# Optimization experiments

Measured on AMD Instinct MI355X. Metric: run time of the kernel, lower is better.

The kernel has to match this reference:

```python
import jax, jax.numpy as jnp
import numpy as np

N = 100_000      # nodes
E = 1_600_000    # edges
F_IN = 128       # n_features == conv_dim1..3
F_OUT = 256      # concat_dim
G = 2000         # number of graphs in the batch
EPS = 1e-5       # BatchNorm eps


def _xavier(k, shape):
    fan_in, fan_out = shape[-2], shape[-1]
    lim = float(np.sqrt(6.0 / (fan_in + fan_out)))
    return jax.random.uniform(k, shape, jnp.float32, -lim, lim)


def setup_inputs() -> dict:
    key = jax.random.key(0)
    ks = jax.random.split(key, 8)
    x = jax.random.normal(ks[0], (N, F_IN), jnp.float32)
    edge_index = jax.random.randint(ks[1], (2, E), 0, N, dtype=jnp.int64)
    batch = jnp.sort(jax.random.randint(ks[2], (N,), 0, G, dtype=jnp.int64))
    # layers 1..5: F_IN -> F_IN (stacked), layer 6: F_IN -> F_OUT
    Wi = _xavier(ks[3], (5, F_IN, F_IN))   # ARMA init_weight per layer
    Wr = _xavier(ks[4], (5, F_IN, F_IN))   # ARMA root_weight per layer
    b = jnp.zeros((5, F_IN), jnp.float32)  # ARMA bias per layer
    g = jnp.ones((5, F_IN), jnp.float32)   # BN gamma
    be = jnp.zeros((5, F_IN), jnp.float32) # BN beta
    Wi6 = _xavier(ks[5], (F_IN, F_OUT))
    Wr6 = _xavier(ks[6], (F_IN, F_OUT))
    b6 = jnp.zeros((F_OUT,), jnp.float32)
    g6 = jnp.ones((F_OUT,), jnp.float32)
    be6 = jnp.zeros((F_OUT,), jnp.float32)
    return dict(x=x, edge_index=edge_index, batch=batch, Wi=Wi, Wr=Wr, b=b,
                g=g, be=be, Wi6=Wi6, Wr6=Wr6, b6=b6, g6=g6, be6=be6)


def _arma(x, norm, row, col, Wi_l, Wr_l, b_l):
    # ARMAConv (num_stacks=1, num_layers=1, act=ReLU):
    #   out = ReLU( A_norm @ (x W_init) + x W_root + b )
    h = x @ Wi_l                                           # [N, F_out]
    msg = h[row] * norm[:, None]                           # gather + scale, [E, F_out]
    agg = jax.ops.segment_sum(msg, col, num_segments=N)    # scatter-add
    return jax.nn.relu(agg + x @ Wr_l + b_l)


def _bn(x, gamma, beta):
    # BatchNorm1d, training mode (biased batch variance)
    mu = x.mean(axis=0)
    var = x.var(axis=0)
    return gamma * (x - mu) * jax.lax.rsqrt(var + EPS) + beta


def reference(x, edge_index, batch, Wi, Wr, b, g, be, Wi6, Wr6, b6, g6, be6):
    row, col = edge_index[0], edge_index[1]
    # gcn_norm without self loops: D^-1/2 A D^-1/2 edge weights
    deg = jax.ops.segment_sum(jnp.ones((E,), x.dtype), col, num_segments=N)
    dinv = jnp.where(deg > 0, jax.lax.rsqrt(deg), 0.0)
    norm = dinv[row] * dinv[col]                           # [E]

    h = x
    for l in range(5):  # fixed small layer count
        h = _arma(h, norm, row, col, Wi[l], Wr[l], b[l])   # outer F.relu is idempotent
        h = _bn(h, g[l], be[l])
    h = _arma(h, norm, row, col, Wi6, Wr6, b6)
    h = _bn(h, g6, be6)
    # global_add_pool over graph ids; dropout = identity (deterministic baseline)
    out = jax.ops.segment_sum(h, batch, num_segments=G)    # [G, F_OUT]
    return out
```

## Files before the change

kernel.cpp:

```cpp
#include <hip/hip_runtime.h>

#define Nn 100000
#define NP 100001
#define Ee 1600000
#define Gg 2000
#define EPSf 1e-5f

typedef unsigned short ushort_t;
typedef __attribute__((ext_vector_type(8))) short short8;
typedef __attribute__((ext_vector_type(4))) float f32x4;
typedef __attribute__((ext_vector_type(4))) unsigned u32x4;

__device__ inline float bf2f(unsigned int u) {
    union { unsigned int i; float f; } v; v.i = u << 16; return v.f;
}
__device__ inline unsigned short f2bf(float f) {
    unsigned int x = __float_as_uint(f);
    unsigned int r = (x + 0x7fffu + ((x >> 16) & 1u)) >> 16;
    return (unsigned short)r;
}
__device__ inline int ldidx(const void* a, int i, int i64) {
    return i64 ? (int)((const long long*)a)[i] : ((const int*)a)[i];
}
__device__ inline float ldflt(const void* p, long long i, int f32) {
    return f32 ? ((const float*)p)[i] : bf2f(((const ushort_t*)p)[i]);
}


__global__ void k_flags(const void* gones, const void* ei, int* flags) {
    if (threadIdx.x == 0 && blockIdx.x == 0) {
        unsigned w = *(const unsigned*)gones;
        flags[0] = (w == 0x3F800000u) ? 1 : 0;
        const int* e = (const int*)ei;
        int nz = 0;
        for (int i = 0; i < 256; i++) nz |= e[2 * i + 1];
        flags[1] = nz ? 0 : 1;
    }
}


__global__ void k_hist(const void* __restrict__ ei, int* __restrict__ deg, const int* __restrict__ flags) {
    int i = blockIdx.x * 256 + threadIdx.x;
    if (i < Ee) {
        int c = ldidx(ei, Ee + i, flags[1]);
        atomicAdd(&deg[c], 1);
    }
}

__global__ void k_dinv(const int* __restrict__ deg, float* __restrict__ dinv) {
    int i = blockIdx.x * 256 + threadIdx.x;
    if (i < Nn) { int d = deg[i]; dinv[i] = d > 0 ? rsqrtf((float)d) : 0.f; }
}

__global__ void k_scan1(const int* __restrict__ deg, int* __restrict__ off, int* __restrict__ part) {
    __shared__ int sh[1024];
    int i = blockIdx.x * 1024 + threadIdx.x;
    int v = (i < Nn) ? ((deg[i] + 3) & ~3) : 0;
    sh[threadIdx.x] = v;
    __syncthreads();
    for (int ofs = 1; ofs < 1024; ofs <<= 1) {
        int t = 0;
        if ((int)threadIdx.x >= ofs) t = sh[threadIdx.x - ofs];
        __syncthreads();
        sh[threadIdx.x] += t;
        __syncthreads();
    }
    if (i < Nn) off[i] = sh[threadIdx.x] - v;
    if (threadIdx.x == 1023) part[blockIdx.x] = sh[1023];
}

__global__ void k_scan2(int* part, int nb) {
    if (threadIdx.x == 0 && blockIdx.x == 0) {
        int run = 0;
        for (int i = 0; i < nb; i++) { int t = part[i]; part[i] = run; run += t; }
        part[nb] = run;
    }
}

__global__ void k_scan3(int* __restrict__ off, const int* __restrict__ part, int* __restrict__ cursor) {
    int i = blockIdx.x * 256 + threadIdx.x;
    if (i < Nn) {
        int v = off[i] + part[i >> 10];
        off[i] = v;
        cursor[i] = v;
    }
    if (i == 0) off[Nn] = part[98];
}

__global__ void k_fillp(const void* __restrict__ ei, int* __restrict__ cursor,
                        int* __restrict__ srcS, const int* __restrict__ flags) {
    int range = blockIdx.x & 7;
    int e = (blockIdx.x >> 3) * 256 + threadIdx.x;
    if (e < Ee) {
        int i64 = flags[1];
        int c = ldidx(ei, Ee + e, i64);
        if (c >= range * 12500 && c < (range + 1) * 12500) {
            int r = ldidx(ei, e, i64);
            int p = atomicAdd(&cursor[c], 1);
            srcS[p] = r;
        }
    }
}

__global__ void k_pad(const int* __restrict__ cursor, const int* __restrict__ off,
                      int* __restrict__ srcS) {
    int i = blockIdx.x * 256 + threadIdx.x;
    if (i < Nn) {
        int e = off[i + 1];
        for (int p = cursor[i]; p < e; p++) srcS[p] = Nn;
    }
}

__global__ void k_zrow(ushort_t* __restrict__ Hi) {
    int t = threadIdx.x;
    int fc = t >> 4, j = t & 15;
    Hi[((size_t)fc * NP + Nn) * 16 + j] = 0;
}

__global__ void k_cvtp(const void* b, const void* b6, const void* g, const void* g6,
                       const void* be, const void* be6,
                       float* __restrict__ biasF, float* __restrict__ gF,
                       float* __restrict__ beF, const int* __restrict__ flags) {
    int i = blockIdx.x * 256 + threadIdx.x;
    if (i >= 2688) return;
    int grp = i / 896, r = i - grp * 896;
    int f32 = flags[0];
    const void* srcs[6] = { b, b6, g, g6, be, be6 };
    float* dsts[3] = { biasF, gF, beF };
    const void* s = (r < 640) ? srcs[grp * 2] : srcs[grp * 2 + 1];
    int idx = (r < 640) ? r : r - 640;
    dsts[grp][r] = ldflt(s, idx, f32);
}

__global__ void k_cvtx(const void* __restrict__ x, ushort_t* __restrict__ xq, const int* __restrict__ flags) {
    int node = blockIdx.x * 256 + threadIdx.x;
    int fc = blockIdx.y;
    if (node < Nn) {
        union { ushort_t u[16]; u32x4 v[2]; } t;
        if (flags[0]) {
            const float* p = (const float*)x + (size_t)node * 128 + fc * 16;
#pragma unroll
            for (int j = 0; j < 16; j++) t.u[j] = f2bf(p[j]);
        } else {
            const ushort_t* p = (const ushort_t*)x + (size_t)node * 128 + fc * 16;
#pragma unroll
            for (int j = 0; j < 16; j++) t.u[j] = p[j];
        }
        u32x4* d = (u32x4*)(xq + ((size_t)fc * Nn + node) * 16);
        d[0] = t.v[0]; d[1] = t.v[1];
    }
}

__global__ void k_pack(const void* __restrict__ Wi, const void* __restrict__ Wr,
                       const void* __restrict__ Wi6, const void* __restrict__ Wr6,
                       ushort_t* __restrict__ Bp, const int* __restrict__ flags) {
    int idx = blockIdx.x * 256 + threadIdx.x;
    if (idx >= 229376) return;
    int f32 = flags[0];
    if (idx < 163840) {
        int l = idx / 32768, rem = idx - l * 32768;
        int kg = rem / 2048, rem2 = rem - kg * 2048;
        int n = rem2 / 8, j = rem2 - n * 8;
        int k = kg * 8 + j;
        float v = (n < 128) ? ldflt(Wi, (l * 128 + k) * 128 + n, f32)
                            : ldflt(Wr, (l * 128 + k) * 128 + (n - 128), f32);
        Bp[idx] = f2bf(v);
    } else {
        int idx2 = idx - 163840;
        int kg = idx2 / 4096, rem2 = idx2 - kg * 4096;
        int n = rem2 / 8, j = rem2 - n * 8;
        int k = kg * 8 + j;
        float v = (n < 256) ? ldflt(Wi6, k * 256 + n, f32) : ldflt(Wr6, k * 256 + (n - 256), f32);
        Bp[idx] = f2bf(v);
    }
}

__global__ void k_fold(const ushort_t* __restrict__ Bp, const float* __restrict__ stat,
                       const float* __restrict__ gamma, const float* __restrict__ beta,
                       const float* __restrict__ bias,
                       ushort_t* __restrict__ Bp2, float* __restrict__ hcorr, int ncat) {
    __shared__ float red[128];
    int n = blockIdx.x, k = threadIdx.x;
    int fhalf = ncat >> 1;
    float mu = stat[k] * (1.f / Nn);
    float var = stat[128 + k] * (1.f / Nn) - mu * mu;
    float rs = rsqrtf(var + EPSf);
    float s = gamma[k] * rs;
    float h = beta[k] - s * mu;
    size_t idx = ((size_t)(k >> 3) * ncat + n) * 8 + (k & 7);
    float w = bf2f(Bp[idx]);
    Bp2[idx] = f2bf(w * s);
    red[k] = h * w;
    __syncthreads();
    for (int m = 64; m > 0; m >>= 1) { if (k < m) red[k] += red[k + m]; __syncthreads(); }
    if (k == 0) hcorr[n] = red[0] + (n >= fhalf ? bias[n - fhalf] : 0.f);
}

__global__ void k_h0(const float* __restrict__ bias, float* __restrict__ hc, int ncat) {
    int n = blockIdx.x * 256 + threadIdx.x;
    if (n < ncat) hc[n] = n >= (ncat >> 1) ? bias[n - (ncat >> 1)] : 0.f;
}


__global__ __launch_bounds__(256) void k_gemm(
        const ushort_t* __restrict__ Aq,
        const ushort_t* __restrict__ Bp, const float* __restrict__ hcorr,
        const float* __restrict__ dinv,
        ushort_t* __restrict__ Hi, ushort_t* __restrict__ yq, int ncat) {
    __shared__ ushort_t stage[32 * 264];
    const int tid = threadIdx.x, lane = tid & 63, wid = tid >> 6;
    const int q = lane >> 4, l15 = lane & 15;
    const int fhalf = ncat >> 1;
    const int colW = blockIdx.y * 256 + wid * 64;
    const int row0 = blockIdx.x * 64;

    short8 bfr[4][4];
    float hc[4];
#pragma unroll
    for (int kk = 0; kk < 4; kk++) {
        int kg = kk * 4 + q;
#pragma unroll
        for (int ct = 0; ct < 4; ct++)
            bfr[kk][ct] = *(const short8*)(Bp + ((size_t)kg * ncat + colW + ct * 16 + l15) * 8);
    }
#pragma unroll
    for (int ct = 0; ct < 4; ct++) hc[ct] = hcorr[colW + ct * 16 + l15];

    f32x4 acc[4][4];
    f32x4 z; z.x = 0.f; z.y = 0.f; z.z = 0.f; z.w = 0.f;
#pragma unroll
    for (int rt = 0; rt < 4; rt++)
#pragma unroll
        for (int ct = 0; ct < 4; ct++) acc[rt][ct] = z;

#pragma unroll
    for (int kk = 0; kk < 4; kk++) {
        int kg = kk * 4 + q;
        const ushort_t* ap = Aq + (size_t)(kg >> 1) * Nn * 16 + (kg & 1) * 8;
        short8 af[4];
#pragma unroll
        for (int rt = 0; rt < 4; rt++) {
            int node = row0 + rt * 16 + l15;
            if (node >= Nn) node = Nn - 1;
            af[rt] = *(const short8*)(ap + (size_t)node * 16);
        }
#pragma unroll
        for (int rt = 0; rt < 4; rt++)
#pragma unroll
            for (int ct = 0; ct < 4; ct++)
                acc[rt][ct] = __builtin_amdgcn_mfma_f32_16x16x32_bf16(af[rt], bfr[kk][ct], acc[rt][ct], 0, 0, 0);
    }

#pragma unroll
    for (int half = 0; half < 2; half++) {
        __syncthreads();
#pragma unroll
        for (int ct = 0; ct < 4; ct++) {
            int lcol = wid * 64 + ct * 16 + l15;
            bool isHi = (blockIdx.y * 256 + lcol) < fhalf;
#pragma unroll
            for (int rt2 = 0; rt2 < 2; rt2++) {
                int rt = half * 2 + rt2;
#pragma unroll
                for (int r = 0; r < 4; r++) {
                    int grow = row0 + rt * 16 + q * 4 + r;
                    int gr = grow < Nn ? grow : 0;
                    float v = acc[rt][ct][r] + hc[ct];
                    if (isHi) v *= dinv[gr];
                    stage[(rt2 * 16 + q * 4 + r) * 264 + lcol] = f2bf(v);
                }
            }
        }
        __syncthreads();
        for (int chunk = tid; chunk < 512; chunk += 256) {
            int cg = chunk & 15, rl = chunk >> 4;
            int node = row0 + half * 32 + rl;
            if (node < Nn) {
                int gc0 = blockIdx.y * 256 + cg * 16;
                const u32x4* sp = (const u32x4*)&stage[rl * 264 + cg * 16];
                u32x4 v0 = sp[0], v1 = sp[1];
                ushort_t* dst = (gc0 < fhalf)
                    ? Hi + ((size_t)(gc0 >> 4) * NP + node) * 16
                    : yq + ((size_t)((gc0 - fhalf) >> 4) * Nn + node) * 16;
                u32x4* dp = (u32x4*)dst;
                dp[0] = v0; dp[1] = v1;
            }
        }
    }
}


__global__ __launch_bounds__(256) void k_agg8(const int* __restrict__ off, const int* __restrict__ src,
                                              const float* __restrict__ dinv, const unsigned* __restrict__ Hi2,
                                              unsigned* __restrict__ yq, float* __restrict__ stat,
                                              int F, int fcbase) {
    const int tid = threadIdx.x;
    const int w = tid >> 6, lane = tid & 63;
    const int sub = lane >> 3, fl = lane & 7;
    const int e2 = (fl >> 1) & 3;
    const int h  = fl & 1;
    const int fc = fcbase + (blockIdx.x & 7);
    const int T = blockIdx.x >> 3;
    const char* __restrict__ gbase = (const char*)Hi2 + (size_t)fc * ((size_t)NP * 32) + h * 16;

    float stS[8], stQ[8];
#pragma unroll
    for (int j = 0; j < 8; j++) { stS[j] = 0.f; stQ[j] = 0.f; }

#pragma unroll
    for (int pass = 0; pass < 4; pass++) {
        int node = T * 128 + pass * 32 + w * 8 + sub;
        bool valid = node < Nn;
        int p0 = 0, p1 = 0;
        if (valid) { p0 = off[node]; p1 = off[node + 1]; }
        float a[8];
#pragma unroll
        for (int j = 0; j < 8; j++) a[j] = 0.f;
        int p = p0;
        for (; p + 15 < p1; p += 16) {
            int s0 = src[p + e2];
            int s1 = src[p + 4 + e2];
            int s2 = src[p + 8 + e2];
            int s3 = src[p + 12 + e2];
            u32x4 g0 = *(const u32x4*)(gbase + (size_t)((unsigned)s0 << 5));
            u32x4 g1 = *(const u32x4*)(gbase + (size_t)((unsigned)s1 << 5));
            u32x4 g2 = *(const u32x4*)(gbase + (size_t)((unsigned)s2 << 5));
            u32x4 g3 = *(const u32x4*)(gbase + (size_t)((unsigned)s3 << 5));
#pragma unroll
            for (int d = 0; d < 4; d++) {
                a[2*d]   += bf2f(g0[d] & 0xffffu); a[2*d+1] += bf2f(g0[d] >> 16);
                a[2*d]   += bf2f(g1[d] & 0xffffu); a[2*d+1] += bf2f(g1[d] >> 16);
                a[2*d]   += bf2f(g2[d] & 0xffffu); a[2*d+1] += bf2f(g2[d] >> 16);
                a[2*d]   += bf2f(g3[d] & 0xffffu); a[2*d+1] += bf2f(g3[d] >> 16);
            }
        }
        if (p + 7 < p1) {
            int s0 = src[p + e2];
            int s1 = src[p + 4 + e2];
            u32x4 g0 = *(const u32x4*)(gbase + (size_t)((unsigned)s0 << 5));
            u32x4 g1 = *(const u32x4*)(gbase + (size_t)((unsigned)s1 << 5));
#pragma unroll
            for (int d = 0; d < 4; d++) {
                a[2*d]   += bf2f(g0[d] & 0xffffu); a[2*d+1] += bf2f(g0[d] >> 16);
                a[2*d]   += bf2f(g1[d] & 0xffffu); a[2*d+1] += bf2f(g1[d] >> 16);
            }
            p += 8;
        }
        if (p < p1) {
            int s0 = src[p + e2];
            u32x4 g0 = *(const u32x4*)(gbase + (size_t)((unsigned)s0 << 5));
#pragma unroll
            for (int d = 0; d < 4; d++) {
                a[2*d]   += bf2f(g0[d] & 0xffffu); a[2*d+1] += bf2f(g0[d] >> 16);
            }
        }
#pragma unroll
        for (int j = 0; j < 8; j++) {
            a[j] += __shfl_xor(a[j], 2, 64);
            a[j] += __shfl_xor(a[j], 4, 64);
        }
        if (valid && fl < 2) {
            float dv = dinv[node];
            u32x4* yp = (u32x4*)(yq + ((size_t)fc * Nn + node) * 8 + h * 4);
            u32x4 uv = *yp;
#pragma unroll
            for (int d = 0; d < 4; d++) {
                float vlo = fmaxf(bf2f(uv[d] & 0xffffu) + dv * a[2*d],   0.f);
                float vhi = fmaxf(bf2f(uv[d] >> 16)     + dv * a[2*d+1], 0.f);
                uv[d] = (unsigned)f2bf(vlo) | ((unsigned)f2bf(vhi) << 16);
                stS[2*d]   += vlo; stQ[2*d]   += vlo * vlo;
                stS[2*d+1] += vhi; stQ[2*d+1] += vhi * vhi;
            }
            *yp = uv;
        }
    }
#pragma unroll
    for (int j = 0; j < 8; j++) {
        stS[j] += __shfl_xor(stS[j], 8, 64);
        stQ[j] += __shfl_xor(stQ[j], 8, 64);
        stS[j] += __shfl_xor(stS[j], 16, 64);
        stQ[j] += __shfl_xor(stQ[j], 16, 64);
        stS[j] += __shfl_xor(stS[j], 32, 64);
        stQ[j] += __shfl_xor(stQ[j], 32, 64);
    }
    __shared__ float red[4][2][8][2];
    if (lane < 2) {
#pragma unroll
        for (int j = 0; j < 8; j++) {
            red[w][lane][j][0] = stS[j];
            red[w][lane][j][1] = stQ[j];
        }
    }
    __syncthreads();
    if (tid < 32) {
        int hh = tid >> 4, r = tid & 15, j = r >> 1, m = r & 1;
        float s = red[0][hh][j][m] + red[1][hh][j][m] + red[2][hh][j][m] + red[3][hh][j][m];
        int f = fc * 16 + hh * 8 + j;
        atomicAdd(&stat[m * F + f], s);
    }
}


__device__ inline int lb(const void* a, int n, int key, int i64) {
    int lo = 0, hi = n;
    while (lo < hi) { int mid = (lo + hi) >> 1; if (ldidx(a, mid, i64) < key) lo = mid + 1; else hi = mid; }
    return lo;
}

__global__ void k_pool(const ushort_t* __restrict__ y6q, const float* __restrict__ stat,
                       const float* __restrict__ g6, const float* __restrict__ be6,
                       const void* __restrict__ batch, void* __restrict__ out,
                       const int* __restrict__ flags) {
    int g = blockIdx.x;
    int f = threadIdx.x;
    int i64 = flags[1];
    int start = lb(batch, Nn, g, i64);
    int end = lb(batch, Nn, g + 1, i64);
    const ushort_t* yp = y6q + (size_t)(f >> 4) * Nn * 16 + (f & 15);
    float s = 0.f;
    for (int n = start; n < end; n++) s += bf2f(yp[(size_t)n * 16]);
    int cnt = end - start;
    float mu = stat[f] * (1.f / Nn);
    float var = stat[256 + f] * (1.f / Nn) - mu * mu;
    float rs = rsqrtf(var + EPSf);
    float val = g6[f] * rs * (s - (float)cnt * mu) + (float)cnt * be6[f];
    if (flags[0]) ((float*)out)[(size_t)g * 256 + f] = val;
    else          ((ushort_t*)out)[(size_t)g * 256 + f] = f2bf(val);
}


extern "C" void kernel_launch(void* const* d_in, const int* in_sizes, int n_in,
                              void* d_out, int out_size, void* d_ws, size_t ws_size,
                              hipStream_t stream) {
    const void* x    = d_in[0];
    const void* ei   = d_in[1];
    const void* batch= d_in[2];
    const void* Wi   = d_in[3];
    const void* Wr   = d_in[4];
    const void* b    = d_in[5];
    const void* g    = d_in[6];
    const void* be   = d_in[7];
    const void* Wi6  = d_in[8];
    const void* Wr6  = d_in[9];
    const void* b6   = d_in[10];
    const void* g6   = d_in[11];
    const void* be6  = d_in[12];

    char* p = (char*)d_ws;
    auto alloc = [&](size_t bytes) { char* r = p; p += (bytes + 511) & ~(size_t)511; return r; };
    ushort_t* HiB  = (ushort_t*)alloc((size_t)NP * 256 * 2);
    ushort_t* xq   = (ushort_t*)alloc((size_t)Nn * 128 * 2);
    ushort_t* yAq  = (ushort_t*)alloc((size_t)Nn * 128 * 2);
    ushort_t* yBq  = (ushort_t*)alloc((size_t)Nn * 128 * 2);
    ushort_t* y6q  = (ushort_t*)alloc((size_t)Nn * 256 * 2);
    int* srcS      = (int*)alloc(((size_t)Ee + 4 * Nn + 64) * 4);
    int* off       = (int*)alloc((size_t)(Nn + 1) * 4);
    int* cursor    = (int*)alloc((size_t)Nn * 4);
    int* deg       = (int*)alloc((size_t)Nn * 4);
    float* dinv    = (float*)alloc((size_t)Nn * 4);
    int* part      = (int*)alloc(128 * 4);
    float* statsA  = (float*)alloc(6 * 512 * 4);
    ushort_t* Bp   = (ushort_t*)alloc(229376 * 2);
    ushort_t* Bp2  = (ushort_t*)alloc(65536 * 2);
    float* hcorrA  = (float*)alloc(512 * 4);
    int* flags     = (int*)alloc(2 * 4);
    float* biasF   = (float*)alloc(896 * 4);
    float* gF      = (float*)alloc(896 * 4);
    float* beF     = (float*)alloc(896 * 4);
    const unsigned* Hi2 = (const unsigned*)HiB;

    const int AGG_GRID = 782 * 8;
    const int GEMM_GRID = 1563;

    k_flags<<<1, 64, 0, stream>>>(g, ei, flags);
    k_cvtp<<<11, 256, 0, stream>>>(b, b6, g, g6, be, be6, biasF, gF, beF, flags);

    hipMemsetAsync(deg, 0, (size_t)Nn * 4, stream);
    hipMemsetAsync(statsA, 0, 6 * 512 * 4, stream);
    k_hist<<<6250, 256, 0, stream>>>(ei, deg, flags);
    k_dinv<<<391, 256, 0, stream>>>(deg, dinv);
    k_scan1<<<98, 1024, 0, stream>>>(deg, off, part);
    k_scan2<<<1, 64, 0, stream>>>(part, 98);
    k_scan3<<<391, 256, 0, stream>>>(off, part, cursor);
    k_fillp<<<50000, 256, 0, stream>>>(ei, cursor, srcS, flags);
    k_pad<<<391, 256, 0, stream>>>(cursor, off, srcS);
    k_zrow<<<1, 256, 0, stream>>>(HiB);
    k_pack<<<896, 256, 0, stream>>>(Wi, Wr, Wi6, Wr6, Bp, flags);
    k_cvtx<<<dim3(391, 8), 256, 0, stream>>>(x, xq, flags);
    k_h0<<<1, 256, 0, stream>>>(biasF, hcorrA, 256);

    k_gemm<<<dim3(GEMM_GRID, 1), 256, 0, stream>>>(xq, Bp, hcorrA, dinv, HiB, yAq, 256);
    k_agg8<<<AGG_GRID, 256, 0, stream>>>(off, srcS, dinv, Hi2, (unsigned*)yAq, statsA, 128, 0);
    k_fold<<<256, 128, 0, stream>>>(Bp + 32768, statsA, gF, beF, biasF + 128, Bp2, hcorrA, 256);

    k_gemm<<<dim3(GEMM_GRID, 1), 256, 0, stream>>>(yAq, Bp2, hcorrA, dinv, HiB, yBq, 256);
    k_agg8<<<AGG_GRID, 256, 0, stream>>>(off, srcS, dinv, Hi2, (unsigned*)yBq, statsA + 512, 128, 0);
    k_fold<<<256, 128, 0, stream>>>(Bp + 65536, statsA + 512, gF + 128, beF + 128, biasF + 256, Bp2, hcorrA, 256);

    k_gemm<<<dim3(GEMM_GRID, 1), 256, 0, stream>>>(yBq, Bp2, hcorrA, dinv, HiB, yAq, 256);
    k_agg8<<<AGG_GRID, 256, 0, stream>>>(off, srcS, dinv, Hi2, (unsigned*)yAq, statsA + 1024, 128, 0);
    k_fold<<<256, 128, 0, stream>>>(Bp + 98304, statsA + 1024, gF + 256, beF + 256, biasF + 384, Bp2, hcorrA, 256);

    k_gemm<<<dim3(GEMM_GRID, 1), 256, 0, stream>>>(yAq, Bp2, hcorrA, dinv, HiB, yBq, 256);
    k_agg8<<<AGG_GRID, 256, 0, stream>>>(off, srcS, dinv, Hi2, (unsigned*)yBq, statsA + 1536, 128, 0);
    k_fold<<<256, 128, 0, stream>>>(Bp + 131072, statsA + 1536, gF + 384, beF + 384, biasF + 512, Bp2, hcorrA, 256);

    k_gemm<<<dim3(GEMM_GRID, 1), 256, 0, stream>>>(yBq, Bp2, hcorrA, dinv, HiB, yAq, 256);
    k_agg8<<<AGG_GRID, 256, 0, stream>>>(off, srcS, dinv, Hi2, (unsigned*)yAq, statsA + 2048, 128, 0);
    k_fold<<<512, 128, 0, stream>>>(Bp + 163840, statsA + 2048, gF + 512, beF + 512, biasF + 640, Bp2, hcorrA, 512);

    k_gemm<<<dim3(GEMM_GRID, 2), 256, 0, stream>>>(yAq, Bp2, hcorrA, dinv, HiB, y6q, 512);
    k_agg8<<<AGG_GRID, 256, 0, stream>>>(off, srcS, dinv, Hi2, (unsigned*)y6q, statsA + 2560, 256, 0);
    k_agg8<<<AGG_GRID, 256, 0, stream>>>(off, srcS, dinv, Hi2, (unsigned*)y6q, statsA + 2560, 256, 8);
    k_pool<<<Gg, 256, 0, stream>>>(y6q, statsA + 2560, gF + 640, be6 ? beF + 640 : beF + 640, batch, d_out, flags);
}
```

Before: 1.145 ms.

## Sort nodes by degree bucket to balance aggregation warp workloads

Adds a counting sort of nodes into 64 degree buckets, highest degree first, and builds the CSR in that sorted slot order. The aggregation kernel then walks slots and maps each back to its node through a permutation. The goal is to cut divergence inside the 8-node groups of a wavefront, where lanes with short edge lists sit idle waiting for neighbours with long ones. In exchange there are three extra setup kernels, an indirect perm lookup in every aggregation pass, and node writes that are no longer coalesced.

After: 1.182 ms. 3.3% more time.

```diff
diff --git a/kernel.cpp b/kernel.cpp
--- a/kernel.cpp
+++ b/kernel.cpp
@@ -5,6 +5,8 @@
 #define Ee 1600000
 #define Gg 2000
 #define EPSf 1e-5f
+#define NBLK 391
+#define BH_STRIDE 400
 
 typedef unsigned short ushort_t;
 typedef __attribute__((ext_vector_type(8))) short short8;
@@ -25,6 +27,7 @@
 __device__ inline float ldflt(const void* p, long long i, int f32) {
     return f32 ? ((const float*)p)[i] : bf2f(((const ushort_t*)p)[i]);
 }
+__device__ inline int dbucket(int d) { int b = (d + 3) >> 2; return b > 63 ? 63 : b; }
 
 
 __global__ void k_flags(const void* gones, const void* ei, int* flags) {
@@ -52,10 +55,60 @@
     if (i < Nn) { int d = deg[i]; dinv[i] = d > 0 ? rsqrtf((float)d) : 0.f; }
 }
 
-__global__ void k_scan1(const int* __restrict__ deg, int* __restrict__ off, int* __restrict__ part) {
+
+__global__ void k_dhist(const int* __restrict__ deg, int* __restrict__ bhT) {
+    __shared__ int hist[64];
+    int tid = threadIdx.x, blk = blockIdx.x;
+    if (tid < 64) hist[tid] = 0;
+    __syncthreads();
+    int i = blk * 256 + tid;
+    if (i < Nn) atomicAdd(&hist[dbucket(deg[i])], 1);
+    __syncthreads();
+    if (tid < 64) bhT[tid * BH_STRIDE + blk] = hist[tid];
+}
+
+__global__ void k_bscan(int* __restrict__ bhT, int* __restrict__ baseG) {
+    __shared__ int tot[64];
+    __shared__ int base[64];
+    int t = threadIdx.x;
+    int run = 0;
+    for (int k = 0; k < NBLK; k++) {
+        int v = bhT[t * BH_STRIDE + k];
+        bhT[t * BH_STRIDE + k] = run;
+        run += v;
+    }
+    tot[t] = run;
+    __syncthreads();
+    if (t == 0) {
+        int r = 0;
+        for (int b = 63; b >= 0; b--) { base[b] = r; r += tot[b]; }
+    }
+    __syncthreads();
+    baseG[t] = base[t];
+}
+
+__global__ void k_dfill(const int* __restrict__ deg, const float* __restrict__ dinv,
+                        const int* __restrict__ bhT, const int* __restrict__ baseG,
+                        int* __restrict__ perm, int* __restrict__ degS, float* __restrict__ dinvS) {
+    __shared__ int cur[64];
+    int tid = threadIdx.x, blk = blockIdx.x;
+    if (tid < 64) cur[tid] = bhT[tid * BH_STRIDE + blk] + baseG[tid];
+    __syncthreads();
+    int i = blk * 256 + tid;
+    if (i < Nn) {
+        int d = deg[i];
+        int b = dbucket(d);
+        int pos = atomicAdd(&cur[b], 1);
+        perm[pos] = i;
+        degS[pos] = (d + 3) & ~3;
+        dinvS[pos] = dinv[i];
+    }
+}
+
+__global__ void k_scan1(const int* __restrict__ degS, int* __restrict__ off, int* __restrict__ part) {
     __shared__ int sh[1024];
     int i = blockIdx.x * 1024 + threadIdx.x;
-    int v = (i < Nn) ? ((deg[i] + 3) & ~3) : 0;
+    int v = (i < Nn) ? degS[i] : 0;
     sh[threadIdx.x] = v;
     __syncthreads();
     for (int ofs = 1; ofs < 1024; ofs <<= 1) {
@@ -77,14 +130,15 @@
     }
 }
 
-__global__ void k_scan3(int* __restrict__ off, const int* __restrict__ part, int* __restrict__ cursor) {
+__global__ void k_scan3(int* __restrict__ offS, const int* __restrict__ part,
+                        const int* __restrict__ perm, int* __restrict__ cursor) {
     int i = blockIdx.x * 256 + threadIdx.x;
     if (i < Nn) {
-        int v = off[i] + part[i >> 10];
-        off[i] = v;
-        cursor[i] = v;
-    }
-    if (i == 0) off[Nn] = part[98];
+        int v = offS[i] + part[i >> 10];
+        offS[i] = v;
+        cursor[perm[i]] = v;
+    }
+    if (i == 0) offS[Nn] = part[98];
 }
 
 __global__ void k_fillp(const void* __restrict__ ei, int* __restrict__ cursor,
@@ -102,12 +156,13 @@
     }
 }
 
-__global__ void k_pad(const int* __restrict__ cursor, const int* __restrict__ off,
-                      int* __restrict__ srcS) {
+__global__ void k_pad(const int* __restrict__ cursor, const int* __restrict__ offS,
+                      const int* __restrict__ perm, int* __restrict__ srcS) {
     int i = blockIdx.x * 256 + threadIdx.x;
     if (i < Nn) {
-        int e = off[i + 1];
-        for (int p = cursor[i]; p < e; p++) srcS[p] = Nn;
+        int node = perm[i];
+        int e = offS[i + 1];
+        for (int p = cursor[node]; p < e; p++) srcS[p] = Nn;
     }
 }
 
@@ -290,8 +345,9 @@
 }
 
 
-__global__ __launch_bounds__(256) void k_agg8(const int* __restrict__ off, const int* __restrict__ src,
-                                              const float* __restrict__ dinv, const unsigned* __restrict__ Hi2,
+__global__ __launch_bounds__(256) void k_agg8(const int* __restrict__ offS, const int* __restrict__ src,
+                                              const int* __restrict__ perm,
+                                              const float* __restrict__ dinvS, const unsigned* __restrict__ Hi2,
                                               unsigned* __restrict__ yq, float* __restrict__ stat,
                                               int F, int fcbase) {
     const int tid = threadIdx.x;
@@ -309,10 +365,10 @@
 
 #pragma unroll
     for (int pass = 0; pass < 4; pass++) {
-        int node = T * 128 + pass * 32 + w * 8 + sub;
-        bool valid = node < Nn;
+        int slot = T * 128 + pass * 32 + w * 8 + sub;
+        bool valid = slot < Nn;
         int p0 = 0, p1 = 0;
-        if (valid) { p0 = off[node]; p1 = off[node + 1]; }
+        if (valid) { p0 = offS[slot]; p1 = offS[slot + 1]; }
         float a[8];
 #pragma unroll
         for (int j = 0; j < 8; j++) a[j] = 0.f;
@@ -360,7 +416,8 @@
             a[j] += __shfl_xor(a[j], 4, 64);
         }
         if (valid && fl < 2) {
-            float dv = dinv[node];
+            int node = perm[slot];
+            float dv = dinvS[slot];
             u32x4* yp = (u32x4*)(yq + ((size_t)fc * Nn + node) * 8 + h * 4);
             u32x4 uv = *yp;
 #pragma unroll
@@ -454,7 +511,7 @@
     ushort_t* yBq  = (ushort_t*)alloc((size_t)Nn * 128 * 2);
     ushort_t* y6q  = (ushort_t*)alloc((size_t)Nn * 256 * 2);
     int* srcS      = (int*)alloc(((size_t)Ee + 4 * Nn + 64) * 4);
-    int* off       = (int*)alloc((size_t)(Nn + 1) * 4);
+    int* offS      = (int*)alloc((size_t)(Nn + 1) * 4);
     int* cursor    = (int*)alloc((size_t)Nn * 4);
     int* deg       = (int*)alloc((size_t)Nn * 4);
     float* dinv    = (float*)alloc((size_t)Nn * 4);
@@ -467,6 +524,11 @@
     float* biasF   = (float*)alloc(896 * 4);
     float* gF      = (float*)alloc(896 * 4);
     float* beF     = (float*)alloc(896 * 4);
+    int* perm      = (int*)alloc((size_t)Nn * 4);
+    int* degS      = (int*)alloc((size_t)Nn * 4);
+    float* dinvS   = (float*)alloc((size_t)Nn * 4);
+    int* bhT       = (int*)alloc(64 * BH_STRIDE * 4);
+    int* baseG     = (int*)alloc(64 * 4);
     const unsigned* Hi2 = (const unsigned*)HiB;
 
     const int AGG_GRID = 782 * 8;
@@ -479,38 +541,41 @@
     hipMemsetAsync(statsA, 0, 6 * 512 * 4, stream);
     k_hist<<<6250, 256, 0, stream>>>(ei, deg, flags);
     k_dinv<<<391, 256, 0, stream>>>(deg, dinv);
-    k_scan1<<<98, 1024, 0, stream>>>(deg, off, part);
+    k_dhist<<<NBLK, 256, 0, stream>>>(deg, bhT);
+    k_bscan<<<1, 64, 0, stream>>>(bhT, baseG);
+    k_dfill<<<NBLK, 256, 0, stream>>>(deg, dinv, bhT, baseG, perm, degS, dinvS);
+    k_scan1<<<98, 1024, 0, stream>>>(degS, offS, part);
     k_scan2<<<1, 64, 0, stream>>>(part, 98);
-    k_scan3<<<391, 256, 0, stream>>>(off, part, cursor);
+    k_scan3<<<391, 256, 0, stream>>>(offS, part, perm, cursor);
     k_fillp<<<50000, 256, 0, stream>>>(ei, cursor, srcS, flags);
-    k_pad<<<391, 256, 0, stream>>>(cursor, off, srcS);
+    k_pad<<<391, 256, 0, stream>>>(cursor, offS, perm, srcS);
     k_zrow<<<1, 256, 0, stream>>>(HiB);
     k_pack<<<896, 256, 0, stream>>>(Wi, Wr, Wi6, Wr6, Bp, flags);
     k_cvtx<<<dim3(391, 8), 256, 0, stream>>>(x, xq, flags);
     k_h0<<<1, 256, 0, stream>>>(biasF, hcorrA, 256);
 
     k_gemm<<<dim3(GEMM_GRID, 1), 256, 0, stream>>>(xq, Bp, hcorrA, dinv, HiB, yAq, 256);
-    k_agg8<<<AGG_GRID, 256, 0, stream>>>(off, srcS, dinv, Hi2, (unsigned*)yAq, statsA, 128, 0);
+    k_agg8<<<AGG_GRID, 256, 0, stream>>>(offS, srcS, perm, dinvS, Hi2, (unsigned*)yAq, statsA, 128, 0);
     k_fold<<<256, 128, 0, stream>>>(Bp + 32768, statsA, gF, beF, biasF + 128, Bp2, hcorrA, 256);
 
     k_gemm<<<dim3(GEMM_GRID, 1), 256, 0, stream>>>(yAq, Bp2, hcorrA, dinv, HiB, yBq, 256);
-    k_agg8<<<AGG_GRID, 256, 0, stream>>>(off, srcS, dinv, Hi2, (unsigned*)yBq, statsA + 512, 128, 0);
+    k_agg8<<<AGG_GRID, 256, 0, stream>>>(offS, srcS, perm, dinvS, Hi2, (unsigned*)yBq, statsA + 512, 128, 0);
     k_fold<<<256, 128, 0, stream>>>(Bp + 65536, statsA + 512, gF + 128, beF + 128, biasF + 256, Bp2, hcorrA, 256);
 
     k_gemm<<<dim3(GEMM_GRID, 1), 256, 0, stream>>>(yBq, Bp2, hcorrA, dinv, HiB, yAq, 256);
-    k_agg8<<<AGG_GRID, 256, 0, stream>>>(off, srcS, dinv, Hi2, (unsigned*)yAq, statsA + 1024, 128, 0);
+    k_agg8<<<AGG_GRID, 256, 0, stream>>>(offS, srcS, perm, dinvS, Hi2, (unsigned*)yAq, statsA + 1024, 128, 0);
     k_fold<<<256, 128, 0, stream>>>(Bp + 98304, statsA + 1024, gF + 256, beF + 256, biasF + 384, Bp2, hcorrA, 256);
 
     k_gemm<<<dim3(GEMM_GRID, 1), 256, 0, stream>>>(yAq, Bp2, hcorrA, dinv, HiB, yBq, 256);
-    k_agg8<<<AGG_GRID, 256, 0, stream>>>(off, srcS, dinv, Hi2, (unsigned*)yBq, statsA + 1536, 128, 0);
+    k_agg8<<<AGG_GRID, 256, 0, stream>>>(offS, srcS, perm, dinvS, Hi2, (unsigned*)yBq, statsA + 1536, 128, 0);
     k_fold<<<256, 128, 0, stream>>>(Bp + 131072, statsA + 1536, gF + 384, beF + 384, biasF + 512, Bp2, hcorrA, 256);
 
     k_gemm<<<dim3(GEMM_GRID, 1), 256, 0, stream>>>(yBq, Bp2, hcorrA, dinv, HiB, yAq, 256);
-    k_agg8<<<AGG_GRID, 256, 0, stream>>>(off, srcS, dinv, Hi2, (unsigned*)yAq, statsA + 2048, 128, 0);
+    k_agg8<<<AGG_GRID, 256, 0, stream>>>(offS, srcS, perm, dinvS, Hi2, (unsigned*)yAq, statsA + 2048, 128, 0);
     k_fold<<<512, 128, 0, stream>>>(Bp + 163840, statsA + 2048, gF + 512, beF + 512, biasF + 640, Bp2, hcorrA, 512);
 
     k_gemm<<<dim3(GEMM_GRID, 2), 256, 0, stream>>>(yAq, Bp2, hcorrA, dinv, HiB, y6q, 512);
-    k_agg8<<<AGG_GRID, 256, 0, stream>>>(off, srcS, dinv, Hi2, (unsigned*)y6q, statsA + 2560, 256, 0);
-    k_agg8<<<AGG_GRID, 256, 0, stream>>>(off, srcS, dinv, Hi2, (unsigned*)y6q, statsA + 2560, 256, 8);
-    k_pool<<<Gg, 256, 0, stream>>>(y6q, statsA + 2560, gF + 640, be6 ? beF + 640 : beF + 640, batch, d_out, flags);
-}
+    k_agg8<<<AGG_GRID, 256, 0, stream>>>(offS, srcS, perm, dinvS, Hi2, (unsigned*)y6q, statsA + 2560, 256, 0);
+    k_agg8<<<AGG_GRID, 256, 0, stream>>>(offS, srcS, perm, dinvS, Hi2, (unsigned*)y6q, statsA + 2560, 256, 8);
+    k_pool<<<Gg, 256, 0, stream>>>(y6q, statsA + 2560, gF + 640, beF + 640, batch, d_out, flags);
+}
```

## Aggregate before transform in final layer to halve gather width

Applied to the files above, without the earlier changes.

For the last layer (128→256), the change reorders the algebra: it aggregates the 128-wide input features (pre-scaled by dinv) over neighbors, then runs one K=256 GEMM over [aggregated, root] inputs. This avoids gathering 256-wide transformed features twice, since the old path needed two agg8 passes. The BN shift term is handled through a per-node dsn factor times a folded hm vector, and the BN statistics are now accumulated inside the new GEMM epilogue. It adds a dsn precompute pass, an extra Hs buffer write in layer 5's aggregation, and some changes to the fold and pack layout.

Result: faster. 1.098 ms (-4.1%).

```diff
diff --git a/kernel.cpp b/kernel.cpp
--- a/kernel.cpp
+++ b/kernel.cpp
@@ -50,6 +50,7 @@
 __global__ void k_dinv(const int* __restrict__ deg, float* __restrict__ dinv) {
     int i = blockIdx.x * 256 + threadIdx.x;
     if (i < Nn) { int d = deg[i]; dinv[i] = d > 0 ? rsqrtf((float)d) : 0.f; }
+    if (i == Nn) dinv[i] = 0.f;
 }
 
 __global__ void k_scan1(const int* __restrict__ deg, int* __restrict__ off, int* __restrict__ part) {
@@ -111,10 +112,22 @@
     }
 }
 
-__global__ void k_zrow(ushort_t* __restrict__ Hi) {
+__global__ void k_dsn(const int* __restrict__ off, const int* __restrict__ src,
+                      const float* __restrict__ dinv, float* __restrict__ dsn) {
+    int i = blockIdx.x * 256 + threadIdx.x;
+    if (i < Nn) {
+        int p0 = off[i], p1 = off[i + 1];
+        float s = 0.f;
+        for (int p = p0; p < p1; p++) s += dinv[src[p]];
+        dsn[i] = dinv[i] * s;
+    }
+}
+
+__global__ void k_zrow(ushort_t* __restrict__ Hi, ushort_t* __restrict__ Hs) {
     int t = threadIdx.x;
     int fc = t >> 4, j = t & 15;
     Hi[((size_t)fc * NP + Nn) * 16 + j] = 0;
+    if (t < 128) Hs[((size_t)(t >> 4) * NP + Nn) * 16 + (t & 15)] = 0;
 }
 
 __global__ void k_cvtp(const void* b, const void* b6, const void* g, const void* g6,
@@ -167,10 +180,10 @@
         Bp[idx] = f2bf(v);
     } else {
         int idx2 = idx - 163840;
-        int kg = idx2 / 4096, rem2 = idx2 - kg * 4096;
+        int kg = idx2 / 2048, rem2 = idx2 - kg * 2048;
         int n = rem2 / 8, j = rem2 - n * 8;
         int k = kg * 8 + j;
-        float v = (n < 256) ? ldflt(Wi6, k * 256 + n, f32) : ldflt(Wr6, k * 256 + (n - 256), f32);
+        float v = (k < 128) ? ldflt(Wi6, k * 256 + n, f32) : ldflt(Wr6, (k - 128) * 256 + n, f32);
         Bp[idx] = f2bf(v);
     }
 }
@@ -196,6 +209,34 @@
     if (k == 0) hcorr[n] = red[0] + (n >= fhalf ? bias[n - fhalf] : 0.f);
 }
 
+__global__ void k_fold5(const ushort_t* __restrict__ Braw, const float* __restrict__ stat,
+                        const float* __restrict__ gamma, const float* __restrict__ beta,
+                        const float* __restrict__ bias,
+                        ushort_t* __restrict__ Bf, float* __restrict__ hm, float* __restrict__ hcorr) {
+    __shared__ float redA[128];
+    __shared__ float redB[128];
+    int n = blockIdx.x, k = threadIdx.x;
+    float mu = stat[k] * (1.f / Nn);
+    float var = stat[128 + k] * (1.f / Nn) - mu * mu;
+    float rs = rsqrtf(var + EPSf);
+    float s = gamma[k] * rs;
+    float t = beta[k] - s * mu;
+    size_t idxWi = ((size_t)(k >> 3) * 256 + n) * 8 + (k & 7);
+    size_t idxWr = ((size_t)(16 + (k >> 3)) * 256 + n) * 8 + (k & 7);
+    float wi = bf2f(Braw[idxWi]);
+    float wr = bf2f(Braw[idxWr]);
+    Bf[idxWi] = f2bf(wi * s);
+    Bf[idxWr] = f2bf(wr * s);
+    redA[k] = t * wi;
+    redB[k] = t * wr;
+    __syncthreads();
+    for (int m = 64; m > 0; m >>= 1) {
+        if (k < m) { redA[k] += redA[k + m]; redB[k] += redB[k + m]; }
+        __syncthreads();
+    }
+    if (k == 0) { hm[n] = redA[0]; hcorr[n] = redB[0] + bias[n]; }
+}
+
 __global__ void k_h0(const float* __restrict__ bias, float* __restrict__ hc, int ncat) {
     int n = blockIdx.x * 256 + threadIdx.x;
     if (n < ncat) hc[n] = n >= (ncat >> 1) ? bias[n - (ncat >> 1)] : 0.f;
@@ -211,7 +252,7 @@
     const int tid = threadIdx.x, lane = tid & 63, wid = tid >> 6;
     const int q = lane >> 4, l15 = lane & 15;
     const int fhalf = ncat >> 1;
-    const int colW = blockIdx.y * 256 + wid * 64;
+    const int colW = wid * 64;
     const int row0 = blockIdx.x * 64;
 
     short8 bfr[4][4];
@@ -257,7 +298,7 @@
 #pragma unroll
         for (int ct = 0; ct < 4; ct++) {
             int lcol = wid * 64 + ct * 16 + l15;
-            bool isHi = (blockIdx.y * 256 + lcol) < fhalf;
+            bool isHi = lcol < fhalf;
 #pragma unroll
             for (int rt2 = 0; rt2 < 2; rt2++) {
                 int rt = half * 2 + rt2;
@@ -276,7 +317,7 @@
             int cg = chunk & 15, rl = chunk >> 4;
             int node = row0 + half * 32 + rl;
             if (node < Nn) {
-                int gc0 = blockIdx.y * 256 + cg * 16;
+                int gc0 = cg * 16;
                 const u32x4* sp = (const u32x4*)&stage[rl * 264 + cg * 16];
                 u32x4 v0 = sp[0], v1 = sp[1];
                 ushort_t* dst = (gc0 < fhalf)
@@ -290,10 +331,105 @@
 }
 
 
+__global__ __launch_bounds__(256) void k_gemm5(
+        const ushort_t* __restrict__ aggH, const ushort_t* __restrict__ y4,
+        const ushort_t* __restrict__ Bp, const float* __restrict__ hcorr,
+        const float* __restrict__ hm, const float* __restrict__ dsn,
+        ushort_t* __restrict__ y6, float* __restrict__ stat) {
+    __shared__ ushort_t stage[32 * 264];
+    const int tid = threadIdx.x, lane = tid & 63, wid = tid >> 6;
+    const int q = lane >> 4, l15 = lane & 15;
+    const int colW = wid * 64;
+    const int row0 = blockIdx.x * 64;
+
+    float hc[4], hmv[4];
+#pragma unroll
+    for (int ct = 0; ct < 4; ct++) {
+        hc[ct] = hcorr[colW + ct * 16 + l15];
+        hmv[ct] = hm[colW + ct * 16 + l15];
+    }
+
+    f32x4 acc[4][4];
+    f32x4 z; z.x = 0.f; z.y = 0.f; z.z = 0.f; z.w = 0.f;
+#pragma unroll
+    for (int rt = 0; rt < 4; rt++)
+#pragma unroll
+        for (int ct = 0; ct < 4; ct++) acc[rt][ct] = z;
+
+#pragma unroll
+    for (int kk = 0; kk < 8; kk++) {
+        int kg = kk * 4 + q;
+        const ushort_t* ap = ((kg < 16)
+            ? aggH + (size_t)(kg >> 1) * ((size_t)Nn * 16)
+            : y4 + (size_t)((kg - 16) >> 1) * ((size_t)Nn * 16)) + (kg & 1) * 8;
+        short8 af[4];
+#pragma unroll
+        for (int rt = 0; rt < 4; rt++) {
+            int node = row0 + rt * 16 + l15;
+            if (node >= Nn) node = Nn - 1;
+            af[rt] = *(const short8*)(ap + (size_t)node * 16);
+        }
+        short8 bf[4];
+#pragma unroll
+        for (int ct = 0; ct < 4; ct++)
+            bf[ct] = *(const short8*)(Bp + ((size_t)kg * 256 + colW + ct * 16 + l15) * 8);
+#pragma unroll
+        for (int rt = 0; rt < 4; rt++)
+#pragma unroll
+            for (int ct = 0; ct < 4; ct++)
+                acc[rt][ct] = __builtin_amdgcn_mfma_f32_16x16x32_bf16(af[rt], bf[ct], acc[rt][ct], 0, 0, 0);
+    }
+
+    float sS = 0.f, sQ = 0.f;
+#pragma unroll
+    for (int half = 0; half < 2; half++) {
+        __syncthreads();
+#pragma unroll
+        for (int ct = 0; ct < 4; ct++) {
+            int lcol = wid * 64 + ct * 16 + l15;
+#pragma unroll
+            for (int rt2 = 0; rt2 < 2; rt2++) {
+                int rt = half * 2 + rt2;
+#pragma unroll
+                for (int r = 0; r < 4; r++) {
+                    int grow = row0 + rt * 16 + q * 4 + r;
+                    int gr = grow < Nn ? grow : 0;
+                    float v = acc[rt][ct][r] + hc[ct] + dsn[gr] * hmv[ct];
+                    v = fmaxf(v, 0.f);
+                    stage[(rt2 * 16 + q * 4 + r) * 264 + lcol] = f2bf(v);
+                }
+            }
+        }
+        __syncthreads();
+        for (int chunk = tid; chunk < 512; chunk += 256) {
+            int cg = chunk & 15, rl = chunk >> 4;
+            int node = row0 + half * 32 + rl;
+            if (node < Nn) {
+                int gc0 = cg * 16;
+                const u32x4* sp = (const u32x4*)&stage[rl * 264 + cg * 16];
+                u32x4 v0 = sp[0], v1 = sp[1];
+                ushort_t* dst = y6 + ((size_t)(gc0 >> 4) * Nn + node) * 16;
+                u32x4* dp = (u32x4*)dst;
+                dp[0] = v0; dp[1] = v1;
+            }
+        }
+        for (int rl = 0; rl < 32; rl++) {
+            int node = row0 + half * 32 + rl;
+            if (node < Nn) {
+                float v = bf2f(stage[rl * 264 + tid]);
+                sS += v; sQ += v * v;
+            }
+        }
+    }
+    atomicAdd(&stat[tid], sS);
+    atomicAdd(&stat[256 + tid], sQ);
+}
+
+
 __global__ __launch_bounds__(256) void k_agg8(const int* __restrict__ off, const int* __restrict__ src,
                                               const float* __restrict__ dinv, const unsigned* __restrict__ Hi2,
                                               unsigned* __restrict__ yq, float* __restrict__ stat,
-                                              int F, int fcbase) {
+                                              int F, int fcbase, unsigned* __restrict__ HsOut) {
     const int tid = threadIdx.x;
     const int w = tid >> 6, lane = tid & 63;
     const int sub = lane >> 3, fl = lane & 7;
@@ -363,15 +499,18 @@
             float dv = dinv[node];
             u32x4* yp = (u32x4*)(yq + ((size_t)fc * Nn + node) * 8 + h * 4);
             u32x4 uv = *yp;
+            u32x4 hs;
 #pragma unroll
             for (int d = 0; d < 4; d++) {
                 float vlo = fmaxf(bf2f(uv[d] & 0xffffu) + dv * a[2*d],   0.f);
                 float vhi = fmaxf(bf2f(uv[d] >> 16)     + dv * a[2*d+1], 0.f);
                 uv[d] = (unsigned)f2bf(vlo) | ((unsigned)f2bf(vhi) << 16);
+                hs[d] = (unsigned)f2bf(vlo * dv) | ((unsigned)f2bf(vhi * dv) << 16);
                 stS[2*d]   += vlo; stQ[2*d]   += vlo * vlo;
                 stS[2*d+1] += vhi; stQ[2*d+1] += vhi * vhi;
             }
             *yp = uv;
+            if (HsOut) *(u32x4*)(HsOut + ((size_t)fc * NP + node) * 8 + h * 4) = hs;
         }
     }
 #pragma unroll
@@ -397,6 +536,82 @@
         float s = red[0][hh][j][m] + red[1][hh][j][m] + red[2][hh][j][m] + red[3][hh][j][m];
         int f = fc * 16 + hh * 8 + j;
         atomicAdd(&stat[m * F + f], s);
+    }
+}
+
+
+__global__ __launch_bounds__(256) void k_agg5(const int* __restrict__ off, const int* __restrict__ src,
+                                              const float* __restrict__ dinv, const unsigned* __restrict__ Hs2,
+                                              unsigned* __restrict__ aggH) {
+    const int tid = threadIdx.x;
+    const int w = tid >> 6, lane = tid & 63;
+    const int sub = lane >> 3, fl = lane & 7;
+    const int e2 = (fl >> 1) & 3;
+    const int h  = fl & 1;
+    const int fc = blockIdx.x & 7;
+    const int T = blockIdx.x >> 3;
+    const char* __restrict__ gbase = (const char*)Hs2 + (size_t)fc * ((size_t)NP * 32) + h * 16;
+
+#pragma unroll
+    for (int pass = 0; pass < 4; pass++) {
+        int node = T * 128 + pass * 32 + w * 8 + sub;
+        bool valid = node < Nn;
+        int p0 = 0, p1 = 0;
+        if (valid) { p0 = off[node]; p1 = off[node + 1]; }
+        float a[8];
+#pragma unroll
+        for (int j = 0; j < 8; j++) a[j] = 0.f;
+        int p = p0;
+        for (; p + 15 < p1; p += 16) {
+            int s0 = src[p + e2];
+            int s1 = src[p + 4 + e2];
+            int s2 = src[p + 8 + e2];
+            int s3 = src[p + 12 + e2];
+            u32x4 g0 = *(const u32x4*)(gbase + (size_t)((unsigned)s0 << 5));
+            u32x4 g1 = *(const u32x4*)(gbase + (size_t)((unsigned)s1 << 5));
+            u32x4 g2 = *(const u32x4*)(gbase + (size_t)((unsigned)s2 << 5));
+            u32x4 g3 = *(const u32x4*)(gbase + (size_t)((unsigned)s3 << 5));
+#pragma unroll
+            for (int d = 0; d < 4; d++) {
+                a[2*d]   += bf2f(g0[d] & 0xffffu); a[2*d+1] += bf2f(g0[d] >> 16);
+                a[2*d]   += bf2f(g1[d] & 0xffffu); a[2*d+1] += bf2f(g1[d] >> 16);
+                a[2*d]   += bf2f(g2[d] & 0xffffu); a[2*d+1] += bf2f(g2[d] >> 16);
+                a[2*d]   += bf2f(g3[d] & 0xffffu); a[2*d+1] += bf2f(g3[d] >> 16);
+            }
+        }
+        if (p + 7 < p1) {
+            int s0 = src[p + e2];
+            int s1 = src[p + 4 + e2];
+            u32x4 g0 = *(const u32x4*)(gbase + (size_t)((unsigned)s0 << 5));
+            u32x4 g1 = *(const u32x4*)(gbase + (size_t)((unsigned)s1 << 5));
+#pragma unroll
+            for (int d = 0; d < 4; d++) {
+                a[2*d]   += bf2f(g0[d] & 0xffffu); a[2*d+1] += bf2f(g0[d] >> 16);
+                a[2*d]   += bf2f(g1[d] & 0xffffu); a[2*d+1] += bf2f(g1[d] >> 16);
+            }
+            p += 8;
+        }
+        if (p < p1) {
+            int s0 = src[p + e2];
+            u32x4 g0 = *(const u32x4*)(gbase + (size_t)((unsigned)s0 << 5));
+#pragma unroll
+            for (int d = 0; d < 4; d++) {
+                a[2*d]   += bf2f(g0[d] & 0xffffu); a[2*d+1] += bf2f(g0[d] >> 16);
+            }
+        }
+#pragma unroll
+        for (int j = 0; j < 8; j++) {
+            a[j] += __shfl_xor(a[j], 2, 64);
+            a[j] += __shfl_xor(a[j], 4, 64);
+        }
+        if (valid && fl < 2) {
+            float dv = dinv[node];
+            u32x4 o;
+#pragma unroll
+            for (int d = 0; d < 4; d++)
+                o[d] = (unsigned)f2bf(dv * a[2*d]) | ((unsigned)f2bf(dv * a[2*d+1]) << 16);
+            *(u32x4*)(aggH + ((size_t)fc * Nn + node) * 8 + h * 4) = o;
+        }
     }
 }
 
@@ -449,6 +664,8 @@
     char* p = (char*)d_ws;
     auto alloc = [&](size_t bytes) { char* r = p; p += (bytes + 511) & ~(size_t)511; return r; };
     ushort_t* HiB  = (ushort_t*)alloc((size_t)NP * 256 * 2);
+    ushort_t* HsB  = (ushort_t*)alloc((size_t)NP * 128 * 2);
+    ushort_t* aggH = (ushort_t*)alloc((size_t)Nn * 128 * 2);
     ushort_t* xq   = (ushort_t*)alloc((size_t)Nn * 128 * 2);
     ushort_t* yAq  = (ushort_t*)alloc((size_t)Nn * 128 * 2);
     ushort_t* yBq  = (ushort_t*)alloc((size_t)Nn * 128 * 2);
@@ -457,12 +674,15 @@
     int* off       = (int*)alloc((size_t)(Nn + 1) * 4);
     int* cursor    = (int*)alloc((size_t)Nn * 4);
     int* deg       = (int*)alloc((size_t)Nn * 4);
-    float* dinv    = (float*)alloc((size_t)Nn * 4);
+    float* dinv    = (float*)alloc((size_t)(Nn + 1) * 4);
+    float* dsn     = (float*)alloc((size_t)Nn * 4);
     int* part      = (int*)alloc(128 * 4);
     float* statsA  = (float*)alloc(6 * 512 * 4);
     ushort_t* Bp   = (ushort_t*)alloc(229376 * 2);
     ushort_t* Bp2  = (ushort_t*)alloc(65536 * 2);
     float* hcorrA  = (float*)alloc(512 * 4);
+    float* hm6     = (float*)alloc(256 * 4);
+    float* hcorr6  = (float*)alloc(256 * 4);
     int* flags     = (int*)alloc(2 * 4);
     float* biasF   = (float*)alloc(896 * 4);
     float* gF      = (float*)alloc(896 * 4);
@@ -478,39 +698,39 @@
     hipMemsetAsync(deg, 0, (size_t)Nn * 4, stream);
     hipMemsetAsync(statsA, 0, 6 * 512 * 4, stream);
     k_hist<<<6250, 256, 0, stream>>>(ei, deg, flags);
-    k_dinv<<<391, 256, 0, stream>>>(deg, dinv);
+    k_dinv<<<392, 256, 0, stream>>>(deg, dinv);
     k_scan1<<<98, 1024, 0, stream>>>(deg, off, part);
     k_scan2<<<1, 64, 0, stream>>>(part, 98);
     k_scan3<<<391, 256, 0, stream>>>(off, part, cursor);
     k_fillp<<<50000, 256, 0, stream>>>(ei, cursor, srcS, flags);
     k_pad<<<391, 256, 0, stream>>>(cursor, off, srcS);
-    k_zrow<<<1, 256, 0, stream>>>(HiB);
+    k_dsn<<<391, 256, 0, stream>>>(off, srcS, dinv, dsn);
+    k_zrow<<<1, 256, 0, stream>>>(HiB, HsB);
     k_pack<<<896, 256, 0, stream>>>(Wi, Wr, Wi6, Wr6, Bp, flags);
     k_cvtx<<<dim3(391, 8), 256, 0, stream>>>(x, xq, flags);
     k_h0<<<1, 256, 0, stream>>>(biasF, hcorrA, 256);
 
     k_gemm<<<dim3(GEMM_GRID, 1), 256, 0, stream>>>(xq, Bp, hcorrA, dinv, HiB, yAq, 256);
-    k_agg8<<<AGG_GRID, 256, 0, stream>>>(off, srcS, dinv, Hi2, (unsigned*)yAq, statsA, 128, 0);
+    k_agg8<<<AGG_GRID, 256, 0, stream>>>(off, srcS, dinv, Hi2, (unsigned*)yAq, statsA, 128, 0, nullptr);
     k_fold<<<256, 128, 0, stream>>>(Bp + 32768, statsA, gF, beF, biasF + 128, Bp2, hcorrA, 256);
 
     k_gemm<<<dim3(GEMM_GRID, 1), 256, 0, stream>>>(yAq, Bp2, hcorrA, dinv, HiB, yBq, 256);
-    k_agg8<<<AGG_GRID, 256, 0, stream>>>(off, srcS, dinv, Hi2, (unsigned*)yBq, statsA + 512, 128, 0);
+    k_agg8<<<AGG_GRID, 256, 0, stream>>>(off, srcS, dinv, Hi2, (unsigned*)yBq, statsA + 512, 128, 0, nullptr);
     k_fold<<<256, 128, 0, stream>>>(Bp + 65536, statsA + 512, gF + 128, beF + 128, biasF + 256, Bp2, hcorrA, 256);
 
     k_gemm<<<dim3(GEMM_GRID, 1), 256, 0, stream>>>(yBq, Bp2, hcorrA, dinv, HiB, yAq, 256);
-    k_agg8<<<AGG_GRID, 256, 0, stream>>>(off, srcS, dinv, Hi2, (unsigned*)yAq, statsA + 1024, 128, 0);
+    k_agg8<<<AGG_GRID, 256, 0, stream>>>(off, srcS, dinv, Hi2, (unsigned*)yAq, statsA + 1024, 128, 0, nullptr);
     k_fold<<<256, 128, 0, stream>>>(Bp + 98304, statsA + 1024, gF + 256, beF + 256, biasF + 384, Bp2, hcorrA, 256);
 
     k_gemm<<<dim3(GEMM_GRID, 1), 256, 0, stream>>>(yAq, Bp2, hcorrA, dinv, HiB, yBq, 256);
-    k_agg8<<<AGG_GRID, 256, 0, stream>>>(off, srcS, dinv, Hi2, (unsigned*)yBq, statsA + 1536, 128, 0);
+    k_agg8<<<AGG_GRID, 256, 0, stream>>>(off, srcS, dinv, Hi2, (unsigned*)yBq, statsA + 1536, 128, 0, nullptr);
     k_fold<<<256, 128, 0, stream>>>(Bp + 131072, statsA + 1536, gF + 384, beF + 384, biasF + 512, Bp2, hcorrA, 256);
 
     k_gemm<<<dim3(GEMM_GRID, 1), 256, 0, stream>>>(yBq, Bp2, hcorrA, dinv, HiB, yAq, 256);
-    k_agg8<<<AGG_GRID, 256, 0, stream>>>(off, srcS, dinv, Hi2, (unsigned*)yAq, statsA + 2048, 128, 0);
-    k_fold<<<512, 128, 0, stream>>>(Bp + 163840, statsA + 2048, gF + 512, beF + 512, biasF + 640, Bp2, hcorrA, 512);
-
-    k_gemm<<<dim3(GEMM_GRID, 2), 256, 0, stream>>>(yAq, Bp2, hcorrA, dinv, HiB, y6q, 512);
-    k_agg8<<<AGG_GRID, 256, 0, stream>>>(off, srcS, dinv, Hi2, (unsigned*)y6q, statsA + 2560, 256, 0);
-    k_agg8<<<AGG_GRID, 256, 0, stream>>>(off, srcS, dinv, Hi2, (unsigned*)y6q, statsA + 2560, 256, 8);
-    k_pool<<<Gg, 256, 0, stream>>>(y6q, statsA + 2560, gF + 640, be6 ? beF + 640 : beF + 640, batch, d_out, flags);
-}
+    k_agg8<<<AGG_GRID, 256, 0, stream>>>(off, srcS, dinv, Hi2, (unsigned*)yAq, statsA + 2048, 128, 0, (unsigned*)HsB);
+
+    k_fold5<<<256, 128, 0, stream>>>(Bp + 163840, statsA + 2048, gF + 512, beF + 512, biasF + 640, Bp2, hm6, hcorr6);
+    k_agg5<<<AGG_GRID, 256, 0, stream>>>(off, srcS, dinv, (const unsigned*)HsB, (unsigned*)aggH);
+    k_gemm5<<<GEMM_GRID, 256, 0, stream>>>(aggH, yAq, Bp2, hcorr6, hm6, dsn, y6q, statsA + 2560);
+    k_pool<<<Gg, 256, 0, stream>>>(y6q, statsA + 2560, gF + 640, beF + 640, batch, d_out, flags);
+}
```
